# Kernel optimization log

Hardware: AMD Instinct MI355X
Metric: run time of the kernel (lower is better)

Reference implementation:

```python
import jax, jax.numpy as jnp
import numpy as np

D_MODEL = 1024
N_HEADS = 16
D_K = 64
D_V = 64
B = 2
S = 2048


def setup_inputs() -> dict:
    key = jax.random.key(0)
    ks = jax.random.split(key, 7)
    q = jax.random.normal(ks[0], (B, S, D_MODEL), dtype=jnp.float32)
    k = jax.random.normal(ks[1], (B, S, D_MODEL), dtype=jnp.float32)
    v = jax.random.normal(ks[2], (B, S, D_MODEL), dtype=jnp.float32)
    mask = jnp.ones((B, S, S), dtype=bool)
    sc = 1.0 / np.sqrt(D_MODEL)
    Wq = jax.random.normal(ks[3], (D_MODEL, N_HEADS * D_K), dtype=jnp.float32) * sc
    Wk = jax.random.normal(ks[4], (D_MODEL, N_HEADS * D_K), dtype=jnp.float32) * sc
    Wv = jax.random.normal(ks[5], (D_MODEL, N_HEADS * D_V), dtype=jnp.float32) * sc
    Wo = jax.random.normal(ks[6], (N_HEADS * D_V, D_MODEL), dtype=jnp.float32) * sc
    return {"q": q, "k": k, "v": v, "mask": mask,
            "Wq": Wq, "Wk": Wk, "Wv": Wv, "Wo": Wo}


def reference(q, k, v, mask, Wq, Wk, Wv, Wo):
    # projections (no bias)
    qh = (q @ Wq).reshape(B, S, N_HEADS, D_K).transpose(0, 2, 1, 3)  # [B,H,Sq,dk]
    kh = (k @ Wk).reshape(B, S, N_HEADS, D_K).transpose(0, 2, 1, 3)  # [B,H,Sk,dk]
    vh = (v @ Wv).reshape(B, S, N_HEADS, D_V).transpose(0, 2, 1, 3)  # [B,H,Sk,dv]
    # NOTE: original module does NOT scale by 1/sqrt(d_k)
    scores = jnp.einsum('bhqd,bhkd->bhqk', qh, kh)  # [B,H,Sq,Sk]
    scores = jnp.where(mask[:, None, :, :], scores, -jnp.inf)
    attn = jax.nn.softmax(scores, axis=-1)
    # dropout p=0.0 -> identity (eval mode)
    out = jnp.einsum('bhqk,bhkd->bhqd', attn, vh)  # [B,H,Sq,dv]
    out = out.transpose(0, 2, 1, 3).reshape(B, S, N_HEADS * D_V)
    return out @ Wo  # [B,S,d_model]
```

## Files before the change

kernel.cpp:

```cpp
#include <hip/hip_runtime.h>

typedef _Float16 half_t;
typedef _Float16 half8 __attribute__((ext_vector_type(8)));
typedef _Float16 half4 __attribute__((ext_vector_type(4)));
typedef float f32x4 __attribute__((ext_vector_type(4)));
typedef short short4v __attribute__((ext_vector_type(4)));
typedef unsigned int uint2v __attribute__((ext_vector_type(2)));
typedef unsigned int uint4v __attribute__((ext_vector_type(4)));
typedef unsigned short ushort4v __attribute__((ext_vector_type(4)));
typedef unsigned short ushort8 __attribute__((ext_vector_type(8)));
typedef __bf16 bf16x8_t __attribute__((ext_vector_type(8)));

#define LOG2E 1.4426950408889634f

#define MFMA32_BF16(A, B, C) __builtin_amdgcn_mfma_f32_16x16x32_bf16((A), (B), (C), 0, 0, 0)

__device__ __forceinline__ void gl2lds16(const void* g, void* l) {
    __builtin_amdgcn_global_load_lds(
        (const __attribute__((address_space(1))) void*)g,
        (__attribute__((address_space(3))) void*)l, 16, 0, 0);
}

__device__ __forceinline__ unsigned pk_bf16(float a, float b) {
    unsigned ua = __builtin_bit_cast(unsigned, a) + 0x8000u;
    unsigned ub = __builtin_bit_cast(unsigned, b) + 0x8000u;
    return __builtin_amdgcn_perm(ub, ua, 0x07060302u);
}

__device__ __forceinline__ unsigned short bf16_bits(float a) {
    return (unsigned short)((__builtin_bit_cast(unsigned, a) + 0x8000u) >> 16);
}

__global__ __launch_bounds__(256) void prep_kernel(
    const float* __restrict__ q, const float* __restrict__ k,
    const float* __restrict__ v,
    const float* __restrict__ W0, const float* __restrict__ W1,
    const float* __restrict__ W2, const float* __restrict__ W3,
    half_t* __restrict__ X, half_t* __restrict__ WqkvT, half_t* __restrict__ WoT)
{
    __shared__ __attribute__((aligned(16))) float T[64][65];
    const int bid = blockIdx.x;
    if (bid < 12288) {
        size_t t = (size_t)bid * 256 + threadIdx.x;
        size_t e = t * 4;
        int id = (int)(e >> 22);
        const float* src = (id == 0) ? q : (id == 1) ? k : v;
        size_t off = e & ((1u << 22) - 1);
        float4 f = *(const float4*)(src + off);
        half4 hv = { (half_t)f.x, (half_t)f.y, (half_t)f.z, (half_t)f.w };
        *(half4*)(X + e) = hv;
        return;
    }
    const int bid2 = bid - 12288;
    const int z = bid2 >> 8;
    const int y = (bid2 >> 4) & 15;
    const int x = bid2 & 15;
    const float* W = (z == 0) ? W0 : (z == 1) ? W1 : (z == 2) ? W2 : W3;
    half_t* D = (z == 0) ? WqkvT : (z == 1) ? WqkvT + 1048576
              : (z == 2) ? WqkvT + 2097152 : WoT;
    const float sc = (z == 0) ? LOG2E : 1.0f;
    const int r0 = y * 64;
    const int c0 = x * 64;
    const int tid = threadIdx.x;
    const int tr = tid >> 4;
    const int tc = (tid & 15) * 4;
#pragma unroll
    for (int p = 0; p < 4; ++p) {
        int r = p * 16 + tr;
        float4 f = *(const float4*)(W + (size_t)(r0 + r) * 1024 + c0 + tc);
        T[r][tc + 0] = f.x; T[r][tc + 1] = f.y; T[r][tc + 2] = f.z; T[r][tc + 3] = f.w;
    }
    __syncthreads();
#pragma unroll
    for (int p = 0; p < 4; ++p) {
        int n = p * 16 + tr;
        half4 hv = { (half_t)(T[tc + 0][n] * sc), (half_t)(T[tc + 1][n] * sc),
                     (half_t)(T[tc + 2][n] * sc), (half_t)(T[tc + 3][n] * sc) };
        *(half4*)(D + (size_t)(c0 + n) * 1024 + r0 + tc) = hv;
    }
}

__global__ __launch_bounds__(256) void gemm_qkv_kernel(
    const half_t* __restrict__ A,
    const half_t* __restrict__ Bt0, const half_t* __restrict__ Bt1,
    const half_t* __restrict__ Bt2,
    half_t* __restrict__ C, unsigned short* __restrict__ VhtOut)
{
    __shared__ __attribute__((aligned(16))) char smem[32768];
    const int tid = threadIdx.x;
    const int lane = tid & 63;
    const int w = tid >> 6;
    const int quad = lane >> 4;
    const int l16 = lane & 15;
    const int wm = w >> 1, wn = w & 1;
    const int swz4 = l16 & 3;
    const int N = 1024;

    const int m0 = blockIdx.x * 128;
    const int n0 = blockIdx.y * 128;
    const int slab = blockIdx.x >> 5;
    const half_t* Bt = (slab == 0) ? Bt0 : (slab == 1) ? Bt1 : Bt2;

    int cA0 = tid, cA1 = tid + 256;
    const half_t* gA0 = A + (size_t)(m0 + (cA0 >> 2)) * 1024 + (((cA0 & 3) ^ ((cA0 >> 2) & 3)) * 8);
    const half_t* gA1 = A + (size_t)(m0 + (cA1 >> 2)) * 1024 + (((cA1 & 3) ^ ((cA1 >> 2) & 3)) * 8);
    const half_t* gB0 = Bt + (size_t)(n0 + (cA0 >> 2)) * 1024 + (((cA0 & 3) ^ ((cA0 >> 2) & 3)) * 8);
    const half_t* gB1 = Bt + (size_t)(n0 + (cA1 >> 2)) * 1024 + (((cA1 & 3) ^ ((cA1 >> 2) & 3)) * 8);
    const int lA0 = tid * 16, lA1 = (tid + 256) * 16;
    const int lB0 = 8192 + tid * 16, lB1 = 8192 + (tid + 256) * 16;

    f32x4 acc[4][4] = {};

    gl2lds16(gA0, smem + lA0); gl2lds16(gA1, smem + lA1);
    gl2lds16(gB0, smem + lB0); gl2lds16(gB1, smem + lB1);
    gA0 += 32; gA1 += 32; gB0 += 32; gB1 += 32;

    for (int kt = 0; kt < 32; ++kt) {
        __syncthreads();
        const int cur = (kt & 1) * 16384;
        if (kt < 31) {
            const int nxt = 16384 - cur;
            gl2lds16(gA0, smem + nxt + lA0); gl2lds16(gA1, smem + nxt + lA1);
            gl2lds16(gB0, smem + nxt + lB0); gl2lds16(gB1, smem + nxt + lB1);
            gA0 += 32; gA1 += 32; gB0 += 32; gB1 += 32;
        }
        const half_t* As = (const half_t*)(smem + cur);
        const half_t* Bs = (const half_t*)(smem + cur + 8192);
        half8 af[4], bf[4];
#pragma unroll
        for (int mt = 0; mt < 4; ++mt)
            af[mt] = *(const half8*)&As[(wm * 64 + mt * 16 + l16) * 32 + ((quad ^ swz4) * 8)];
#pragma unroll
        for (int nt = 0; nt < 4; ++nt)
            bf[nt] = *(const half8*)&Bs[(wn * 64 + nt * 16 + l16) * 32 + ((quad ^ swz4) * 8)];
#pragma unroll
        for (int mt = 0; mt < 4; ++mt)
#pragma unroll
            for (int nt = 0; nt < 4; ++nt)
                acc[mt][nt] = __builtin_amdgcn_mfma_f32_16x16x32_f16(
                    af[mt], bf[nt], acc[mt][nt], 0, 0, 0);
    }

    if (slab < 2) {
#pragma unroll
        for (int mt = 0; mt < 4; ++mt) {
            int rbase = m0 + wm * 64 + mt * 16 + quad * 4;
#pragma unroll
            for (int nt = 0; nt < 4; ++nt) {
                int col = n0 + wn * 64 + nt * 16 + l16;
#pragma unroll
                for (int r = 0; r < 4; ++r)
                    C[(size_t)(rbase + r) * N + col] = (half_t)acc[mt][nt][r];
            }
        }
    } else {
        unsigned short* Tr = (unsigned short*)smem;
        const int tok0 = m0 - 8192;
        const int bb = tok0 >> 11;
        const int ss0 = tok0 & 2047;
#pragma unroll
        for (int p = 0; p < 2; ++p) {
            __syncthreads();
#pragma unroll
            for (int t16 = 0; t16 < 2; ++t16) {
                int nt = 2 * p + t16;
                int c = wn * 32 + t16 * 16 + l16;
#pragma unroll
                for (int mt = 0; mt < 4; ++mt) {
                    int sb = wm * 64 + mt * 16 + quad * 4;
                    ushort4v pk = { bf16_bits(acc[mt][nt][0]), bf16_bits(acc[mt][nt][1]),
                                    bf16_bits(acc[mt][nt][2]), bf16_bits(acc[mt][nt][3]) };
                    *(ushort4v*)&Tr[c * 136 + sb] = pk;
                }
            }
            __syncthreads();
            int cc = tid >> 2, seg = tid & 3;
            int colit = ((cc >> 5) << 6) + 32 * p + (cc & 31);
            int ncol = n0 + colit;
            int row_out = ((bb << 4) + (ncol >> 6)) * 64 + (ncol & 63);
            unsigned short* gdst = VhtOut + (size_t)row_out * 2048 + ss0 + seg * 32;
            const unsigned short* lsrc = Tr + cc * 136 + seg * 32;
#pragma unroll
            for (int u = 0; u < 4; ++u)
                *(ushort8*)(gdst + u * 8) = *(const ushort8*)(lsrc + u * 8);
        }
    }
}

__global__ __launch_bounds__(256) void gemm_bt_m64_kernel(
    const half_t* __restrict__ A, const half_t* __restrict__ Bt,
    float* __restrict__ C)
{
    __shared__ __attribute__((aligned(16))) char smem[24576];
    const int tid = threadIdx.x;
    const int lane = tid & 63;
    const int w = tid >> 6;
    const int quad = lane >> 4;
    const int l16 = lane & 15;
    const int wm = w >> 1, wn = w & 1;
    const int swz4 = l16 & 3;
    const int N = 1024;

    const int m0 = blockIdx.x * 64;
    const int n0 = blockIdx.y * 128;

    int c0 = tid, c1 = tid + 256;
    const half_t* gA0 = A + (size_t)(m0 + (c0 >> 2)) * 1024 + (((c0 & 3) ^ ((c0 >> 2) & 3)) * 8);
    const half_t* gB0 = Bt + (size_t)(n0 + (c0 >> 2)) * 1024 + (((c0 & 3) ^ ((c0 >> 2) & 3)) * 8);
    const half_t* gB1 = Bt + (size_t)(n0 + (c1 >> 2)) * 1024 + (((c1 & 3) ^ ((c1 >> 2) & 3)) * 8);
    const int lA0 = tid * 16;
    const int lB0 = 4096 + tid * 16, lB1 = 4096 + (tid + 256) * 16;

    f32x4 acc[2][4] = {};

    gl2lds16(gA0, smem + lA0);
    gl2lds16(gB0, smem + lB0); gl2lds16(gB1, smem + lB1);
    gA0 += 32; gB0 += 32; gB1 += 32;

    for (int kt = 0; kt < 32; ++kt) {
        __syncthreads();
        const int cur = (kt & 1) * 12288;
        if (kt < 31) {
            const int nxt = 12288 - cur;
            gl2lds16(gA0, smem + nxt + lA0);
            gl2lds16(gB0, smem + nxt + lB0); gl2lds16(gB1, smem + nxt + lB1);
            gA0 += 32; gB0 += 32; gB1 += 32;
        }
        const half_t* As = (const half_t*)(smem + cur);
        const half_t* Bs = (const half_t*)(smem + cur + 4096);
        half8 af[2], bf[4];
#pragma unroll
        for (int mt = 0; mt < 2; ++mt)
            af[mt] = *(const half8*)&As[(wm * 32 + mt * 16 + l16) * 32 + ((quad ^ swz4) * 8)];
#pragma unroll
        for (int nt = 0; nt < 4; ++nt)
            bf[nt] = *(const half8*)&Bs[(wn * 64 + nt * 16 + l16) * 32 + ((quad ^ swz4) * 8)];
#pragma unroll
        for (int mt = 0; mt < 2; ++mt)
#pragma unroll
            for (int nt = 0; nt < 4; ++nt)
                acc[mt][nt] = __builtin_amdgcn_mfma_f32_16x16x32_f16(
                    af[mt], bf[nt], acc[mt][nt], 0, 0, 0);
    }
#pragma unroll
    for (int mt = 0; mt < 2; ++mt) {
        int rbase = m0 + wm * 32 + mt * 16 + quad * 4;
#pragma unroll
        for (int nt = 0; nt < 4; ++nt) {
            int col = n0 + wn * 64 + nt * 16 + l16;
#pragma unroll
            for (int r = 0; r < 4; ++r)
                C[(size_t)(rbase + r) * N + col] = acc[mt][nt][r];
        }
    }
}

__global__ __launch_bounds__(512, 4) void attn_kernel(
    const half_t* __restrict__ Qh, const half_t* __restrict__ Kh,
    const unsigned short* __restrict__ Vht, half_t* __restrict__ Out)
{
    __shared__ __attribute__((aligned(16))) char smem[65536];

    const int tid = threadIdx.x;
    const int lane = tid & 63;
    const int w = tid >> 6;
    const int wq = w & 3;
    const int ws = w >> 2;
    const int quad = lane >> 4;
    const int l16 = lane & 15;
    const int swz = l16 & 7;

    const int bid = blockIdx.x;
    const int bh = bid & 31;
    const int qt = bid >> 5;
    const int h = bh & 15;
    const int b = bh >> 4;
    const int qrow0 = b * 2048 + qt * 128;
    const int qbase = qrow0 + wq * 32;

    half8 qf[2][2];
#pragma unroll
    for (int qg = 0; qg < 2; ++qg)
#pragma unroll
        for (int ks = 0; ks < 2; ++ks)
            qf[qg][ks] = *(const half8*)(Qh + (size_t)(qbase + qg * 16 + l16) * 1024
                                         + h * 64 + ks * 32 + quad * 8);

    const half_t* kp[2]; const unsigned short* vp[2];
    int ldk[2], ldv[2];
#pragma unroll
    for (int i = 0; i < 2; ++i) {
        int c = i * 512 + tid;
        int rK = c >> 3, gK = (c & 7) ^ (rK & 7);
        kp[i] = Kh + (size_t)(b * 2048 + rK) * 1024 + h * 64 + gK * 8;
        ldk[i] = c * 16;
        int rV = c >> 4, gV = (c & 15) ^ (rV & 7);
        vp[i] = Vht + (size_t)(bh * 64 + rV) * 2048 + gV * 8;
        ldv[i] = 16384 + c * 16;
    }

    f32x4 accT[2][4] = {};
    f32x4 accL[2] = {};
    const ushort8 onesu = { 0x3F80, 0x3F80, 0x3F80, 0x3F80,
                            0x3F80, 0x3F80, 0x3F80, 0x3F80 };
    const bf16x8_t ones8 = __builtin_bit_cast(bf16x8_t, onesu);

#pragma unroll
    for (int i = 0; i < 2; ++i) {
        gl2lds16(kp[i], (char*)smem + ldk[i]);
        gl2lds16(vp[i], (char*)smem + ldv[i]);
        kp[i] += 128 * 1024; vp[i] += 128;
    }

    for (int kt = 0; kt < 16; ++kt) {
        __syncthreads();
        const int cur = (kt & 1) * 32768;
        if (kt < 15) {
            const int nxt = 32768 - cur;
#pragma unroll
            for (int i = 0; i < 2; ++i) {
                gl2lds16(kp[i], (char*)smem + nxt + ldk[i]);
                gl2lds16(vp[i], (char*)smem + nxt + ldv[i]);
                kp[i] += 128 * 1024; vp[i] += 128;
            }
        }
        const half_t* Ksp = (const half_t*)(smem + cur);
        const unsigned short* Vsp = (const unsigned short*)(smem + cur + 16384);

        uint4v pbu[2][2];
#pragma unroll
        for (int t = 0; t < 4; ++t) {
            int srow = ws * 64 + t * 16 + l16;
            half8 k0 = *(const half8*)&Ksp[srow * 64 + ((quad ^ swz) * 8)];
            half8 k1 = *(const half8*)&Ksp[srow * 64 + (((4 + quad) ^ swz) * 8)];
#pragma unroll
            for (int qg = 0; qg < 2; ++qg) {
                f32x4 z = {};
                z = __builtin_amdgcn_mfma_f32_16x16x32_f16(k0, qf[qg][0], z, 0, 0, 0);
                z = __builtin_amdgcn_mfma_f32_16x16x32_f16(k1, qf[qg][1], z, 0, 0, 0);
                float e0 = __builtin_amdgcn_exp2f(z[0]);
                float e1 = __builtin_amdgcn_exp2f(z[1]);
                float e2 = __builtin_amdgcn_exp2f(z[2]);
                float e3 = __builtin_amdgcn_exp2f(z[3]);
                pbu[qg][t >> 1][(t & 1) * 2 + 0] = pk_bf16(e0, e1);
                pbu[qg][t >> 1][(t & 1) * 2 + 1] = pk_bf16(e2, e3);
            }
        }

#pragma unroll
        for (int t2 = 0; t2 < 2; ++t2) {
            bf16x8_t p0 = __builtin_bit_cast(bf16x8_t, pbu[0][t2]);
            bf16x8_t p1 = __builtin_bit_cast(bf16x8_t, pbu[1][t2]);
#pragma unroll
            for (int dt = 0; dt < 4; ++dt) {
                int row = dt * 16 + l16;
                int gA = ws * 8 + t2 * 4 + (quad >> 1);
                uint2v vA = *(const uint2v*)&Vsp[row * 128 + ((gA ^ swz) << 3) + (quad & 1) * 4];
                uint2v vB = *(const uint2v*)&Vsp[row * 128 + (((gA + 2) ^ swz) << 3) + (quad & 1) * 4];
                uint4v vv = { vA[0], vA[1], vB[0], vB[1] };
                bf16x8_t vf = __builtin_bit_cast(bf16x8_t, vv);
                accT[0][dt] = MFMA32_BF16(vf, p0, accT[0][dt]);
                accT[1][dt] = MFMA32_BF16(vf, p1, accT[1][dt]);
            }
            accL[0] = MFMA32_BF16(ones8, p0, accL[0]);
            accL[1] = MFMA32_BF16(ones8, p1, accL[1]);
        }
    }

    __syncthreads();
    float* RB = (float*)smem;
    float* RL = (float*)(smem + 32768);
    if (w >= 4) {
        int wb = w - 4;
#pragma unroll
        for (int qg = 0; qg < 2; ++qg) {
#pragma unroll
            for (int dt = 0; dt < 4; ++dt)
                *(f32x4*)&RB[(((wb * 2 + qg) * 4 + dt) << 8) + lane * 4] = accT[qg][dt];
            RL[((wb * 2 + qg) << 6) + lane] = accL[qg][0];
        }
    }
    __syncthreads();
    float sum0 = 0.0f, sum1 = 0.0f;
    if (w < 4) {
#pragma unroll
        for (int qg = 0; qg < 2; ++qg)
#pragma unroll
            for (int dt = 0; dt < 4; ++dt)
                accT[qg][dt] += *(const f32x4*)&RB[(((w * 2 + qg) * 4 + dt) << 8) + lane * 4];
        sum0 = accL[0][0] + RL[((w * 2 + 0) << 6) + lane];
        sum1 = accL[1][0] + RL[((w * 2 + 1) << 6) + lane];
    }
    __syncthreads();

    if (w < 4) {
        float inv0 = 1.0f / sum0;
        float inv1 = 1.0f / sum1;
        half_t* Ob = (half_t*)smem + w * (32 * 72);
#pragma unroll
        for (int qg = 0; qg < 2; ++qg) {
            float iv = qg ? inv1 : inv0;
#pragma unroll
            for (int dt = 0; dt < 4; ++dt) {
                f32x4 a = accT[qg][dt];
                half4 hv = { (half_t)(a[0] * iv), (half_t)(a[1] * iv),
                             (half_t)(a[2] * iv), (half_t)(a[3] * iv) };
                *(half4*)&Ob[(qg * 16 + l16) * 72 + dt * 16 + quad * 4] = hv;
            }
        }
    }
    __syncthreads();
    if (w < 4) {
        half_t* Ob = (half_t*)smem + w * (32 * 72);
#pragma unroll
        for (int p = 0; p < 4; ++p) {
            int cid = p * 64 + lane;
            int row = cid >> 3, ch = cid & 7;
            half8 vv = *(const half8*)&Ob[row * 72 + ch * 8];
            *(half8*)(Out + (size_t)(qbase + row) * 1024 + h * 64 + ch * 8) = vv;
        }
    }
}

extern "C" void kernel_launch(void* const* d_in, const int* in_sizes, int n_in,
                              void* d_out, int out_size, void* d_ws, size_t ws_size,
                              hipStream_t stream)
{
    const float* q  = (const float*)d_in[0];
    const float* k  = (const float*)d_in[1];
    const float* v  = (const float*)d_in[2];
    const float* Wq = (const float*)d_in[4];
    const float* Wk = (const float*)d_in[5];
    const float* Wv = (const float*)d_in[6];
    const float* Wo = (const float*)d_in[7];
    float* out = (float*)d_out;
    char* ws = (char*)d_ws;

    half_t* Xqkv    = (half_t*)(ws);
    half_t* AttnOut = (half_t*)(ws + 8388608);
    half_t* WqkvT   = (half_t*)(ws + 25165824);
    half_t* WoT     = (half_t*)(ws + 31457280);
    half_t* QKVh    = (half_t*)(ws + 33554432);
    unsigned short* Vht = (unsigned short*)(QKVh + (size_t)8192 * 1024);

    prep_kernel<<<13312, 256, 0, stream>>>(
        q, k, v, Wq, Wk, Wv, Wo, Xqkv, WqkvT, WoT);
    gemm_qkv_kernel<<<dim3(96, 8), 256, 0, stream>>>(
        Xqkv, WqkvT, WqkvT + 1024 * 1024, WqkvT + 2 * 1024 * 1024,
        QKVh, Vht);
    attn_kernel<<<512, 512, 0, stream>>>(
        QKVh, QKVh + (size_t)4096 * 1024, Vht, AttnOut);
    gemm_bt_m64_kernel<<<dim3(64, 8), 256, 0, stream>>>(
        AttnOut, WoT, out);
}
```

Before: 233.4 us.

## Load V directly into registers in pre-permuted layout, drop V LDS staging

The V-transpose producer now writes each 8-element chunk as two interleaved 4-element halves, so the attention kernel can read V fragments straight from global memory into registers with single 16-byte loads. This replaces the V double buffer in shared memory, which shrinks LDS from 64KB to 34KB, removes the split 8-byte LDS reads, and should allow higher occupancy. It also raises wave priority around the PV MFMA block. The cost is that V global-load latency is now exposed inside each iteration with no LDS prefetch to hide it.

```diff
diff --git a/kernel.cpp b/kernel.cpp
--- a/kernel.cpp
+++ b/kernel.cpp
@@ -4,7 +4,6 @@
 typedef _Float16 half8 __attribute__((ext_vector_type(8)));
 typedef _Float16 half4 __attribute__((ext_vector_type(4)));
 typedef float f32x4 __attribute__((ext_vector_type(4)));
-typedef short short4v __attribute__((ext_vector_type(4)));
 typedef unsigned int uint2v __attribute__((ext_vector_type(2)));
 typedef unsigned int uint4v __attribute__((ext_vector_type(4)));
 typedef unsigned short ushort4v __attribute__((ext_vector_type(4)));
@@ -181,8 +180,12 @@
             unsigned short* gdst = VhtOut + (size_t)row_out * 2048 + ss0 + seg * 32;
             const unsigned short* lsrc = Tr + cc * 136 + seg * 32;
 #pragma unroll
-            for (int u = 0; u < 4; ++u)
-                *(ushort8*)(gdst + u * 8) = *(const ushort8*)(lsrc + u * 8);
+            for (int u = 0; u < 4; ++u) {
+                ushort4v lo = *(const ushort4v*)(lsrc + u * 4);
+                ushort4v hi = *(const ushort4v*)(lsrc + u * 4 + 16);
+                ushort8 o = { lo[0], lo[1], lo[2], lo[3], hi[0], hi[1], hi[2], hi[3] };
+                *(ushort8*)(gdst + u * 8) = o;
+            }
         }
     }
 }
@@ -259,7 +262,7 @@
     const half_t* __restrict__ Qh, const half_t* __restrict__ Kh,
     const unsigned short* __restrict__ Vht, half_t* __restrict__ Out)
 {
-    __shared__ __attribute__((aligned(16))) char smem[65536];
+    __shared__ __attribute__((aligned(16))) char smem[34816];
 
     const int tid = threadIdx.x;
     const int lane = tid & 63;
@@ -286,18 +289,17 @@
             qf[qg][ks] = *(const half8*)(Qh + (size_t)(qbase + qg * 16 + l16) * 1024
                                          + h * 64 + ks * 32 + quad * 8);
 
-    const half_t* kp[2]; const unsigned short* vp[2];
-    int ldk[2], ldv[2];
+    const half_t* kp[2];
+    int ldk[2];
 #pragma unroll
     for (int i = 0; i < 2; ++i) {
         int c = i * 512 + tid;
         int rK = c >> 3, gK = (c & 7) ^ (rK & 7);
         kp[i] = Kh + (size_t)(b * 2048 + rK) * 1024 + h * 64 + gK * 8;
         ldk[i] = c * 16;
-        int rV = c >> 4, gV = (c & 15) ^ (rV & 7);
-        vp[i] = Vht + (size_t)(bh * 64 + rV) * 2048 + gV * 8;
-        ldv[i] = 16384 + c * 16;
-    }
+    }
+
+    const unsigned short* Vrow = Vht + (size_t)(bh * 64 + l16) * 2048 + quad * 8;
 
     f32x4 accT[2][4] = {};
     f32x4 accL[2] = {};
@@ -308,24 +310,30 @@
 #pragma unroll
     for (int i = 0; i < 2; ++i) {
         gl2lds16(kp[i], (char*)smem + ldk[i]);
-        gl2lds16(vp[i], (char*)smem + ldv[i]);
-        kp[i] += 128 * 1024; vp[i] += 128;
+        kp[i] += 128 * 1024;
     }
 
     for (int kt = 0; kt < 16; ++kt) {
         __syncthreads();
-        const int cur = (kt & 1) * 32768;
+        const int cur = (kt & 1) * 16384;
+
+        uint4v vreg[2][4];
+        const unsigned short* vb = Vrow + (kt * 4 + ws * 2) * 32;
+#pragma unroll
+        for (int t2 = 0; t2 < 2; ++t2)
+#pragma unroll
+            for (int dt = 0; dt < 4; ++dt)
+                vreg[t2][dt] = *(const uint4v*)(vb + t2 * 32 + dt * 32768);
+
         if (kt < 15) {
-            const int nxt = 32768 - cur;
+            const int nxt = 16384 - cur;
 #pragma unroll
             for (int i = 0; i < 2; ++i) {
                 gl2lds16(kp[i], (char*)smem + nxt + ldk[i]);
-                gl2lds16(vp[i], (char*)smem + nxt + ldv[i]);
-                kp[i] += 128 * 1024; vp[i] += 128;
+                kp[i] += 128 * 1024;
             }
         }
         const half_t* Ksp = (const half_t*)(smem + cur);
-        const unsigned short* Vsp = (const unsigned short*)(smem + cur + 16384);
 
         uint4v pbu[2][2];
 #pragma unroll
@@ -347,24 +355,21 @@
             }
         }
 
+        __builtin_amdgcn_s_setprio(1);
 #pragma unroll
         for (int t2 = 0; t2 < 2; ++t2) {
             bf16x8_t p0 = __builtin_bit_cast(bf16x8_t, pbu[0][t2]);
             bf16x8_t p1 = __builtin_bit_cast(bf16x8_t, pbu[1][t2]);
 #pragma unroll
             for (int dt = 0; dt < 4; ++dt) {
-                int row = dt * 16 + l16;
-                int gA = ws * 8 + t2 * 4 + (quad >> 1);
-                uint2v vA = *(const uint2v*)&Vsp[row * 128 + ((gA ^ swz) << 3) + (quad & 1) * 4];
-                uint2v vB = *(const uint2v*)&Vsp[row * 128 + (((gA + 2) ^ swz) << 3) + (quad & 1) * 4];
-                uint4v vv = { vA[0], vA[1], vB[0], vB[1] };
-                bf16x8_t vf = __builtin_bit_cast(bf16x8_t, vv);
+                bf16x8_t vf = __builtin_bit_cast(bf16x8_t, vreg[t2][dt]);
                 accT[0][dt] = MFMA32_BF16(vf, p0, accT[0][dt]);
                 accT[1][dt] = MFMA32_BF16(vf, p1, accT[1][dt]);
             }
             accL[0] = MFMA32_BF16(ones8, p0, accL[0]);
             accL[1] = MFMA32_BF16(ones8, p1, accL[1]);
         }
+        __builtin_amdgcn_s_setprio(0);
     }
 
     __syncthreads();
```

New measurement: 264.2 us. 13.2% more time.
